# Kernel optimization log

Measured on AMD Instinct MI355X. Metric: run time of the kernel, lower is better.

Reference implementation:

```python
import jax, jax.numpy as jnp
import numpy as np

# Per-layer (in_dim, hidden) for the 6 stacked LSTM layers:
# rnn_inp: (1,64),(64,64),(64,64); rnn_out: (64,1),(1,1),(1,1)
_LAYER_DIMS = [(1, 64), (64, 64), (64, 64), (64, 1), (1, 1), (1, 1)]
_LAYER_NAMES = ['a0', 'a1', 'a2', 'b0', 'b1', 'b2']


def _lstm_layer(x, w_ih, w_hh, b_ih, b_hh):
    """Single unidirectional LSTM layer, PyTorch gate order (i, f, g, o).
    x: [B, T, Din]; w_ih: [4H, Din]; w_hh: [4H, H]; biases: [4H]. Returns [B, T, H]."""
    H = w_hh.shape[1]
    B = x.shape[0]
    # Input projection for all timesteps at once (one big GEMM).
    pre = jnp.einsum('btd,gd->btg', x, w_ih) + b_ih + b_hh  # [B, T, 4H]
    pre_t = jnp.swapaxes(pre, 0, 1)  # [T, B, 4H]

    def step(carry, xt):
        h, c = carry
        gates = xt + h @ w_hh.T  # [B, 4H]
        i, f, g, o = jnp.split(gates, 4, axis=-1)
        i = jax.nn.sigmoid(i)
        f = jax.nn.sigmoid(f)
        g = jnp.tanh(g)
        o = jax.nn.sigmoid(o)
        c = f * c + i * g
        h = o * jnp.tanh(c)
        return (h, c), h

    h0 = jnp.zeros((B, H), x.dtype)
    (_, _), hs = jax.lax.scan(step, (h0, h0), pre_t)  # hs: [T, B, H]
    return jnp.swapaxes(hs, 0, 1)


def setup_inputs() -> dict:
    key = jax.random.key(0)
    B, T = 256, 512
    inp = {}
    k, key = jax.random.split(key)
    inp['x'] = jax.random.normal(k, (B, T, 1), dtype=jnp.float32)
    for name, (din, h) in zip(_LAYER_NAMES, _LAYER_DIMS):
        s = 1.0 / np.sqrt(h)  # PyTorch LSTM init scale U(-1/sqrt(H), 1/sqrt(H))
        k1, k2, k3, k4, key = jax.random.split(key, 5)
        inp[f'w_ih_{name}'] = jax.random.uniform(k1, (4 * h, din), jnp.float32, -s, s)
        inp[f'w_hh_{name}'] = jax.random.uniform(k2, (4 * h, h), jnp.float32, -s, s)
        inp[f'b_ih_{name}'] = jax.random.uniform(k3, (4 * h,), jnp.float32, -s, s)
        inp[f'b_hh_{name}'] = jax.random.uniform(k4, (4 * h,), jnp.float32, -s, s)
    return inp


def reference(x,
              w_ih_a0, w_hh_a0, b_ih_a0, b_hh_a0,
              w_ih_a1, w_hh_a1, b_ih_a1, b_hh_a1,
              w_ih_a2, w_hh_a2, b_ih_a2, b_hh_a2,
              w_ih_b0, w_hh_b0, b_ih_b0, b_hh_b0,
              w_ih_b1, w_hh_b1, b_ih_b1, b_hh_b1,
              w_ih_b2, w_hh_b2, b_ih_b2, b_hh_b2):
    layers = [
        (w_ih_a0, w_hh_a0, b_ih_a0, b_hh_a0),
        (w_ih_a1, w_hh_a1, b_ih_a1, b_hh_a1),
        (w_ih_a2, w_hh_a2, b_ih_a2, b_hh_a2),
        (w_ih_b0, w_hh_b0, b_ih_b0, b_hh_b0),
        (w_ih_b1, w_hh_b1, b_ih_b1, b_hh_b1),
        (w_ih_b2, w_hh_b2, b_ih_b2, b_hh_b2),
    ]
    h = x
    for w_ih, w_hh, b_ih, b_hh in layers:
        h = _lstm_layer(h, w_ih, w_hh, b_ih, b_hh)
    # activation between the two LSTM stacks is identity (activation_type='identity')
    return h  # [B, T, 1]
```

## Files before the change

kernel.cpp:

```cpp
#include <hip/hip_runtime.h>


#define BB 256
#define TT 512
#define CH 4
#define NS 16
#define NW (TT / CH)
#define HP 72
#define PP 260

typedef _Float16 v2h __attribute__((ext_vector_type(2)));
typedef _Float16 v8h __attribute__((ext_vector_type(8)));
typedef float v4f __attribute__((ext_vector_type(4)));

__device__ __forceinline__ float sig_(float x) {
  return __builtin_amdgcn_rcpf(1.f + __builtin_amdgcn_exp2f(-1.44269504f * x));
}
__device__ __forceinline__ float tanh_(float x) {
  return __builtin_fmaf(2.f, __builtin_amdgcn_rcpf(1.f + __builtin_amdgcn_exp2f(-2.88539008f * x)), -1.f);
}

template <int K>
__device__ __forceinline__ float qb_(float v) {
  return __int_as_float(__builtin_amdgcn_update_dpp(
      0, __float_as_int(v), (K | (K << 2) | (K << 4) | (K << 6)), 0xF, 0xF, true));
}

#if __has_builtin(__builtin_amdgcn_fdot2)
#define FDOT2(acc, a, b) (acc) = __builtin_amdgcn_fdot2((a), (b), (acc), false)
#else
#define FDOT2(acc, a, b) \
  (acc) = __builtin_fmaf((float)(a)[0], (float)(b)[0], \
          __builtin_fmaf((float)(a)[1], (float)(b)[1], (acc)))
#endif
#define KEEPP(a) asm volatile("" : "+v"(a))
#define PIN16(w)                                                            \
  do {                                                                      \
    _Pragma("unroll") for (int _i = 0; _i < 16; ++_i) KEEPP((w)[_i]);       \
  } while (0)

#define WAITP(i, v)                                                           \
  while (__hip_atomic_load(&prog[i], __ATOMIC_ACQUIRE,                        \
                           __HIP_MEMORY_SCOPE_WORKGROUP) < (v)) {             \
    __builtin_amdgcn_s_sleep(1);                                              \
  }
#define POSTP(i, v)                                                           \
  do {                                                                        \
    asm volatile("s_waitcnt lgkmcnt(0)" ::: "memory");                        \
    if (lane == 0)                                                            \
      __hip_atomic_store(&prog[i], (v), __ATOMIC_RELEASE,                     \
                         __HIP_MEMORY_SCOPE_WORKGROUP);                       \
  } while (0)

__device__ __forceinline__ v2h bc2h_(int v) { return __builtin_bit_cast(v2h, v); }

__device__ __forceinline__ void load_h64(const _Float16* p, v2h hv[32]) {
  const int4* hp = reinterpret_cast<const int4*>(p);
#pragma unroll
  for (int i = 0; i < 8; ++i) {
    int4 blk = hp[i];
    hv[4 * i + 0] = bc2h_(blk.x);
    hv[4 * i + 1] = bc2h_(blk.y);
    hv[4 * i + 2] = bc2h_(blk.z);
    hv[4 * i + 3] = bc2h_(blk.w);
  }
}

__device__ __forceinline__ void load_row_pair(const float* src, v2h* lo, v2h* hi) {
  const float4* p = reinterpret_cast<const float4*>(src);
#pragma unroll
  for (int i = 0; i < 8; ++i) {
    float4 v = p[i];
    lo[2 * i]     = v2h{(_Float16)v.x, (_Float16)v.y};
    lo[2 * i + 1] = v2h{(_Float16)v.z, (_Float16)v.w};
  }
#pragma unroll
  for (int i = 0; i < 8; ++i) {
    float4 v = p[8 + i];
    hi[2 * i]     = v2h{(_Float16)v.x, (_Float16)v.y};
    hi[2 * i + 1] = v2h{(_Float16)v.z, (_Float16)v.w};
  }
}

__device__ __forceinline__ v8h ldbfrag_(const float* W, int t, int kc, int lane) {
  const int row = 16 * t + (lane & 15);
  const float* p = W + row * 64 + 32 * kc + 4 * (lane >> 4);
  float4 fa = *reinterpret_cast<const float4*>(p);
  float4 fb = *reinterpret_cast<const float4*>(p + 16);
  return v8h{(_Float16)fa.x, (_Float16)fa.y, (_Float16)fa.z, (_Float16)fa.w,
             (_Float16)fb.x, (_Float16)fb.y, (_Float16)fb.z, (_Float16)fb.w};
}

__global__ __attribute__((amdgpu_flat_work_group_size(384, 384),
                          amdgpu_waves_per_eu(2, 2)))
void lstm_pipe_k(
    const float* __restrict__ x,
    const float* __restrict__ wih_a0, const float* __restrict__ whh_a0,
    const float* __restrict__ bih_a0, const float* __restrict__ bhh_a0,
    const float* __restrict__ wih_a1, const float* __restrict__ whh_a1,
    const float* __restrict__ bih_a1, const float* __restrict__ bhh_a1,
    const float* __restrict__ wih_a2, const float* __restrict__ whh_a2,
    const float* __restrict__ bih_a2, const float* __restrict__ bhh_a2,
    const float* __restrict__ wih_b0, const float* __restrict__ whh_b0,
    const float* __restrict__ bih_b0, const float* __restrict__ bhh_b0,
    const float* __restrict__ wih_b1, const float* __restrict__ whh_b1,
    const float* __restrict__ bih_b1, const float* __restrict__ bhh_b1,
    const float* __restrict__ wih_b2, const float* __restrict__ whh_b2,
    const float* __restrict__ bih_b2, const float* __restrict__ bhh_b2,
    float* __restrict__ out)
{
  const int b = blockIdx.x;
  const int tid = threadIdx.x;
  const int wave = tid >> 6;
  const int lane = tid & 63;

  __shared__ __align__(16) _Float16 hh[3][NS][HP];
  __shared__ __align__(16) float pj[2][NS][PP];
  __shared__ float xs[TT];
  __shared__ int prog[6];

  for (int i = tid; i < TT; i += 384) xs[i] = x[(size_t)b * TT + i];
  for (int i = tid; i < 3 * NS * HP / 2; i += 384) reinterpret_cast<int*>(hh)[i] = 0;
  if (tid < 6) prog[tid] = 0;

  union UW {
    v8h bfr[16][2];
    v2h wtb[2][16];
  } u;

  float bias[4] = {0.f, 0.f, 0.f, 0.f};
  float wi0_[4] = {0.f, 0.f, 0.f, 0.f};
  float whb0[4] = {}, wi1b[4] = {}, wh1b[4] = {}, bb1[4] = {},
        wi2b[4] = {}, wh2b[4] = {}, bb2[4] = {};

  if (wave == 0) {
#pragma unroll
    for (int t = 0; t < 16; ++t) {
      u.bfr[t][0] = ldbfrag_(whh_a0, t, 0, lane);
      u.bfr[t][1] = ldbfrag_(whh_a0, t, 1, lane);
    }
#pragma unroll
    for (int q = 0; q < 4; ++q) {
      const int row = q * 64 + lane;
      bias[q] = bih_a0[row] + bhh_a0[row];
      wi0_[q] = wih_a0[row];
    }
  } else if (wave == 1) {
#pragma unroll
    for (int t = 0; t < 16; ++t) {
      u.bfr[t][0] = ldbfrag_(whh_a1, t, 0, lane);
      u.bfr[t][1] = ldbfrag_(whh_a1, t, 1, lane);
    }
#pragma unroll
    for (int q = 0; q < 4; ++q) bias[q] = bih_a1[q * 64 + lane] + bhh_a1[q * 64 + lane];
  } else if (wave == 2) {
#pragma unroll
    for (int t = 0; t < 16; ++t) {
      u.bfr[t][0] = ldbfrag_(whh_a2, t, 0, lane);
      u.bfr[t][1] = ldbfrag_(whh_a2, t, 1, lane);
    }
#pragma unroll
    for (int q = 0; q < 4; ++q) bias[q] = bih_a2[q * 64 + lane] + bhh_a2[q * 64 + lane];
  } else if (wave == 3) {
    const int q = lane & 3;
    load_row_pair(wih_b0 + q * 64, u.wtb[0], u.wtb[1]);
    bias[0] = bih_b0[q] + bhh_b0[q];
#pragma unroll
    for (int k = 0; k < 4; ++k) {
      whb0[k] = whh_b0[k];
      wi1b[k] = wih_b1[k]; wh1b[k] = whh_b1[k]; bb1[k] = bih_b1[k] + bhh_b1[k];
      wi2b[k] = wih_b2[k]; wh2b[k] = whh_b2[k]; bb2[k] = bih_b2[k] + bhh_b2[k];
    }
    PIN16(u.wtb[0]); PIN16(u.wtb[1]);
  } else if (wave == 4) {
#pragma unroll
    for (int t = 0; t < 16; ++t) {
      u.bfr[t][0] = ldbfrag_(wih_a1, t, 0, lane);
      u.bfr[t][1] = ldbfrag_(wih_a1, t, 1, lane);
    }
  } else {
#pragma unroll
    for (int t = 0; t < 16; ++t) {
      u.bfr[t][0] = ldbfrag_(wih_a2, t, 0, lane);
      u.bfr[t][1] = ldbfrag_(wih_a2, t, 1, lane);
    }
  }
  __syncthreads();

  float c = 0.f;
  float h0b = 0.f, c0b = 0.f, h1b = 0.f, c1b = 0.f, h2b = 0.f, c2b = 0.f;
  const int q4 = lane >> 4;
  const bool s0 = q4 & 1, s1 = q4 & 2;
  const v4f z = {0.f, 0.f, 0.f, 0.f};

  if (wave == 0) {
    __builtin_amdgcn_s_setprio(1);
    for (int k = 0; k < NW; ++k) {
      if (k >= 4) { WAITP(4, k - 3); }
      const int t0 = k * CH;
      for (int s = 0; s < CH; ++s) {
        const int t = t0 + s;
        const char* hp = (const char*)(&hh[0][(t + NS - 1) & (NS - 1)][0]) + 8 * q4;
        int2 r00 = *(const int2*)(hp);
        int2 r01 = *(const int2*)(hp + 32);
        int2 r10 = *(const int2*)(hp + 64);
        int2 r11 = *(const int2*)(hp + 96);
        v8h A0 = __builtin_bit_cast(v8h, int4{r00.x, r00.y, r01.x, r01.y});
        v8h A1 = __builtin_bit_cast(v8h, int4{r10.x, r10.y, r11.x, r11.y});
        v4f acc[16];
#pragma unroll
        for (int tl = 0; tl < 16; ++tl) {
          v4f d = __builtin_amdgcn_mfma_f32_16x16x32_f16(A0, u.bfr[tl][0], z, 0, 0, 0);
          acc[tl] = __builtin_amdgcn_mfma_f32_16x16x32_f16(A1, u.bfr[tl][1], d, 0, 0, 0);
        }
        float p[4];
#pragma unroll
        for (int g = 0; g < 4; ++g) {
          float v01 = s0 ? acc[4 * g + 1][0] : acc[4 * g + 0][0];
          float v23 = s0 ? acc[4 * g + 3][0] : acc[4 * g + 2][0];
          p[g] = s1 ? v23 : v01;
        }
        const float xv = xs[t];
        float p0 = __builtin_fmaf(wi0_[0], xv, p[0] + bias[0]);
        float p1 = __builtin_fmaf(wi0_[1], xv, p[1] + bias[1]);
        float p2 = __builtin_fmaf(wi0_[2], xv, p[2] + bias[2]);
        float p3 = __builtin_fmaf(wi0_[3], xv, p[3] + bias[3]);
        float gi = sig_(p0), gf = sig_(p1), gg = tanh_(p2), go = sig_(p3);
        c = __builtin_fmaf(gf, c, gi * gg);
        hh[0][t & (NS - 1)][lane] = (_Float16)(go * tanh_(c));
      }
      POSTP(0, k + 1);
    }
    __builtin_amdgcn_s_setprio(0);
  } else if (wave == 1) {
    __builtin_amdgcn_s_setprio(1);
    for (int k = 0; k < NW; ++k) {
      WAITP(4, k + 1);
      if (k >= 4) { WAITP(5, k - 3); }
      const int t0 = k * CH;
      for (int s = 0; s < CH; ++s) {
        const int t = t0 + s;
        const char* hp = (const char*)(&hh[1][(t + NS - 1) & (NS - 1)][0]) + 8 * q4;
        int2 r00 = *(const int2*)(hp);
        int2 r01 = *(const int2*)(hp + 32);
        int2 r10 = *(const int2*)(hp + 64);
        int2 r11 = *(const int2*)(hp + 96);
        v8h A0 = __builtin_bit_cast(v8h, int4{r00.x, r00.y, r01.x, r01.y});
        v8h A1 = __builtin_bit_cast(v8h, int4{r10.x, r10.y, r11.x, r11.y});
        float4 pr = *reinterpret_cast<const float4*>(&pj[0][t & (NS - 1)][lane * 4]);
        v4f acc[16];
#pragma unroll
        for (int tl = 0; tl < 16; ++tl) {
          v4f d = __builtin_amdgcn_mfma_f32_16x16x32_f16(A0, u.bfr[tl][0], z, 0, 0, 0);
          acc[tl] = __builtin_amdgcn_mfma_f32_16x16x32_f16(A1, u.bfr[tl][1], d, 0, 0, 0);
        }
        float p[4];
#pragma unroll
        for (int g = 0; g < 4; ++g) {
          float v01 = s0 ? acc[4 * g + 1][0] : acc[4 * g + 0][0];
          float v23 = s0 ? acc[4 * g + 3][0] : acc[4 * g + 2][0];
          p[g] = s1 ? v23 : v01;
        }
        float p0 = p[0] + bias[0] + pr.x;
        float p1 = p[1] + bias[1] + pr.y;
        float p2 = p[2] + bias[2] + pr.z;
        float p3 = p[3] + bias[3] + pr.w;
        float gi = sig_(p0), gf = sig_(p1), gg = tanh_(p2), go = sig_(p3);
        c = __builtin_fmaf(gf, c, gi * gg);
        hh[1][t & (NS - 1)][lane] = (_Float16)(go * tanh_(c));
      }
      POSTP(1, k + 1);
    }
    __builtin_amdgcn_s_setprio(0);
  } else if (wave == 2) {
    __builtin_amdgcn_s_setprio(1);
    for (int k = 0; k < NW; ++k) {
      WAITP(5, k + 1);
      if (k >= 4) { WAITP(3, k - 3); }
      const int t0 = k * CH;
      for (int s = 0; s < CH; ++s) {
        const int t = t0 + s;
        const char* hp = (const char*)(&hh[2][(t + NS - 1) & (NS - 1)][0]) + 8 * q4;
        int2 r00 = *(const int2*)(hp);
        int2 r01 = *(const int2*)(hp + 32);
        int2 r10 = *(const int2*)(hp + 64);
        int2 r11 = *(const int2*)(hp + 96);
        v8h A0 = __builtin_bit_cast(v8h, int4{r00.x, r00.y, r01.x, r01.y});
        v8h A1 = __builtin_bit_cast(v8h, int4{r10.x, r10.y, r11.x, r11.y});
        float4 pr = *reinterpret_cast<const float4*>(&pj[1][t & (NS - 1)][lane * 4]);
        v4f acc[16];
#pragma unroll
        for (int tl = 0; tl < 16; ++tl) {
          v4f d = __builtin_amdgcn_mfma_f32_16x16x32_f16(A0, u.bfr[tl][0], z, 0, 0, 0);
          acc[tl] = __builtin_amdgcn_mfma_f32_16x16x32_f16(A1, u.bfr[tl][1], d, 0, 0, 0);
        }
        float p[4];
#pragma unroll
        for (int g = 0; g < 4; ++g) {
          float v01 = s0 ? acc[4 * g + 1][0] : acc[4 * g + 0][0];
          float v23 = s0 ? acc[4 * g + 3][0] : acc[4 * g + 2][0];
          p[g] = s1 ? v23 : v01;
        }
        float p0 = p[0] + bias[0] + pr.x;
        float p1 = p[1] + bias[1] + pr.y;
        float p2 = p[2] + bias[2] + pr.z;
        float p3 = p[3] + bias[3] + pr.w;
        float gi = sig_(p0), gf = sig_(p1), gg = tanh_(p2), go = sig_(p3);
        c = __builtin_fmaf(gf, c, gi * gg);
        hh[2][t & (NS - 1)][lane] = (_Float16)(go * tanh_(c));
      }
      POSTP(2, k + 1);
    }
    __builtin_amdgcn_s_setprio(0);
  } else if (wave == 3) {
    for (int k = 0; k < NW; ++k) {
      WAITP(2, k + 1);
      const int t0 = k * CH;
      for (int s = 0; s < CH; ++s) {
        const int t = t0 + s;
        v2h hv[32];
        load_h64(&hh[2][t & (NS - 1)][0], hv);
        float pga = bias[0], pgb = 0.f;
#pragma unroll
        for (int j = 0; j < 16; ++j) {
          FDOT2(pga, u.wtb[0][j], hv[j]);
          FDOT2(pgb, u.wtb[1][j], hv[16 + j]);
        }
        float pg = pga + pgb;
        float p_i = qb_<0>(pg), p_f = qb_<1>(pg), p_g = qb_<2>(pg), p_o = qb_<3>(pg);
        float i0 = sig_(__builtin_fmaf(whb0[0], h0b, p_i));
        float f0 = sig_(__builtin_fmaf(whb0[1], h0b, p_f));
        float g0 = tanh_(__builtin_fmaf(whb0[2], h0b, p_g));
        float o0 = sig_(__builtin_fmaf(whb0[3], h0b, p_o));
        c0b = __builtin_fmaf(f0, c0b, i0 * g0);
        h0b = o0 * tanh_(c0b);
        float i1 = sig_(bb1[0] + __builtin_fmaf(wi1b[0], h0b, wh1b[0] * h1b));
        float f1 = sig_(bb1[1] + __builtin_fmaf(wi1b[1], h0b, wh1b[1] * h1b));
        float g1 = tanh_(bb1[2] + __builtin_fmaf(wi1b[2], h0b, wh1b[2] * h1b));
        float o1 = sig_(bb1[3] + __builtin_fmaf(wi1b[3], h0b, wh1b[3] * h1b));
        c1b = __builtin_fmaf(f1, c1b, i1 * g1);
        h1b = o1 * tanh_(c1b);
        float i2 = sig_(bb2[0] + __builtin_fmaf(wi2b[0], h1b, wh2b[0] * h2b));
        float f2 = sig_(bb2[1] + __builtin_fmaf(wi2b[1], h1b, wh2b[1] * h2b));
        float g2 = tanh_(bb2[2] + __builtin_fmaf(wi2b[2], h1b, wh2b[2] * h2b));
        float o2 = sig_(bb2[3] + __builtin_fmaf(wi2b[3], h1b, wh2b[3] * h2b));
        c2b = __builtin_fmaf(f2, c2b, i2 * g2);
        h2b = o2 * tanh_(c2b);
        if (lane == 0) out[(size_t)b * TT + t] = h2b;
      }
      POSTP(3, k + 1);
    }
  } else if (wave == 4) {
    for (int k = 0; k < NW; ++k) {
      WAITP(0, k + 1);
      if (k >= 4) { WAITP(1, k - 3); }
      const int t0 = k * CH;
      const int slotb = (t0 + (lane & 15)) & (NS - 1);
      const char* hp = (const char*)(&hh[0][slotb][0]) + 8 * q4;
      int2 r00 = *(const int2*)(hp);
      int2 r01 = *(const int2*)(hp + 32);
      int2 r10 = *(const int2*)(hp + 64);
      int2 r11 = *(const int2*)(hp + 96);
      v8h Bf0 = __builtin_bit_cast(v8h, int4{r00.x, r00.y, r01.x, r01.y});
      v8h Bf1 = __builtin_bit_cast(v8h, int4{r10.x, r10.y, r11.x, r11.y});
      float* pbase = &pj[0][slotb][0] + 16 * q4;
      const bool wr = (lane & 15) < CH;
#pragma unroll
      for (int tl = 0; tl < 16; ++tl) {
        v4f acc = __builtin_amdgcn_mfma_f32_16x16x32_f16(u.bfr[tl][0], Bf0, z, 0, 0, 0);
        acc = __builtin_amdgcn_mfma_f32_16x16x32_f16(u.bfr[tl][1], Bf1, acc, 0, 0, 0);
        if (wr) {
          const int o = 64 * (tl & 3) + (tl >> 2);
          pbase[o] = acc[0]; pbase[o + 4] = acc[1];
          pbase[o + 8] = acc[2]; pbase[o + 12] = acc[3];
        }
        __builtin_amdgcn_sched_barrier(0);
      }
      POSTP(4, k + 1);
    }
  } else {
    for (int k = 0; k < NW; ++k) {
      WAITP(1, k + 1);
      if (k >= 4) { WAITP(2, k - 3); }
      const int t0 = k * CH;
      const int slotb = (t0 + (lane & 15)) & (NS - 1);
      const char* hp = (const char*)(&hh[1][slotb][0]) + 8 * q4;
      int2 r00 = *(const int2*)(hp);
      int2 r01 = *(const int2*)(hp + 32);
      int2 r10 = *(const int2*)(hp + 64);
      int2 r11 = *(const int2*)(hp + 96);
      v8h Bf0 = __builtin_bit_cast(v8h, int4{r00.x, r00.y, r01.x, r01.y});
      v8h Bf1 = __builtin_bit_cast(v8h, int4{r10.x, r10.y, r11.x, r11.y});
      float* pbase = &pj[1][slotb][0] + 16 * q4;
      const bool wr = (lane & 15) < CH;
#pragma unroll
      for (int tl = 0; tl < 16; ++tl) {
        v4f acc = __builtin_amdgcn_mfma_f32_16x16x32_f16(u.bfr[tl][0], Bf0, z, 0, 0, 0);
        acc = __builtin_amdgcn_mfma_f32_16x16x32_f16(u.bfr[tl][1], Bf1, acc, 0, 0, 0);
        if (wr) {
          const int o = 64 * (tl & 3) + (tl >> 2);
          pbase[o] = acc[0]; pbase[o + 4] = acc[1];
          pbase[o + 8] = acc[2]; pbase[o + 12] = acc[3];
        }
        __builtin_amdgcn_sched_barrier(0);
      }
      POSTP(5, k + 1);
    }
  }
}

extern "C" void kernel_launch(void* const* d_in, const int* in_sizes, int n_in,
                              void* d_out, int out_size, void* d_ws, size_t ws_size,
                              hipStream_t stream) {
  const float* x      = (const float*)d_in[0];
  const float* wih_a0 = (const float*)d_in[1];
  const float* whh_a0 = (const float*)d_in[2];
  const float* bih_a0 = (const float*)d_in[3];
  const float* bhh_a0 = (const float*)d_in[4];
  const float* wih_a1 = (const float*)d_in[5];
  const float* whh_a1 = (const float*)d_in[6];
  const float* bih_a1 = (const float*)d_in[7];
  const float* bhh_a1 = (const float*)d_in[8];
  const float* wih_a2 = (const float*)d_in[9];
  const float* whh_a2 = (const float*)d_in[10];
  const float* bih_a2 = (const float*)d_in[11];
  const float* bhh_a2 = (const float*)d_in[12];
  const float* wih_b0 = (const float*)d_in[13];
  const float* whh_b0 = (const float*)d_in[14];
  const float* bih_b0 = (const float*)d_in[15];
  const float* bhh_b0 = (const float*)d_in[16];
  const float* wih_b1 = (const float*)d_in[17];
  const float* whh_b1 = (const float*)d_in[18];
  const float* bih_b1 = (const float*)d_in[19];
  const float* bhh_b1 = (const float*)d_in[20];
  const float* wih_b2 = (const float*)d_in[21];
  const float* whh_b2 = (const float*)d_in[22];
  const float* bih_b2 = (const float*)d_in[23];
  const float* bhh_b2 = (const float*)d_in[24];
  float* out = (float*)d_out;

  lstm_pipe_k<<<BB, 384, 0, stream>>>(
      x,
      wih_a0, whh_a0, bih_a0, bhh_a0,
      wih_a1, whh_a1, bih_a1, bhh_a1,
      wih_a2, whh_a2, bih_a2, bhh_a2,
      wih_b0, whh_b0, bih_b0, bhh_b0,
      wih_b1, whh_b1, bih_b1, bhh_b1,
      wih_b2, whh_b2, bih_b2, bhh_b2,
      out);
}
```

Before: 338.4 us.

## Process two batch elements per block to interleave independent recurrences

Each block now handles two batch rows, with shared buffers for hidden states, projections and inputs duplicated per row, and the grid is halved. Recurrent waves issue MFMAs for both rows in an interleaved order so the dependent matmul/activation chain of one row can hide the latency of the other. Projection waves and the scalar tail stage loop over both rows. This trades fewer active CUs and higher register/LDS use for better latency hiding within each wave.

```diff
diff --git a/kernel.cpp b/kernel.cpp
--- a/kernel.cpp
+++ b/kernel.cpp
@@ -1,7 +1,7 @@
 #include <hip/hip_runtime.h>
 
 
-#define BB 256
+#define NB 128
 #define TT 512
 #define CH 4
 #define NS 16
@@ -89,6 +89,58 @@
   float4 fb = *reinterpret_cast<const float4*>(p + 16);
   return v8h{(_Float16)fa.x, (_Float16)fa.y, (_Float16)fa.z, (_Float16)fa.w,
              (_Float16)fb.x, (_Float16)fb.y, (_Float16)fb.z, (_Float16)fb.w};
+}
+
+__device__ __forceinline__ void ldafrag_(const _Float16* hprev, int q4,
+                                         v8h& A0, v8h& A1) {
+  const char* hp = (const char*)hprev + 8 * q4;
+  int2 r00 = *(const int2*)(hp);
+  int2 r01 = *(const int2*)(hp + 32);
+  int2 r10 = *(const int2*)(hp + 64);
+  int2 r11 = *(const int2*)(hp + 96);
+  A0 = __builtin_bit_cast(v8h, int4{r00.x, r00.y, r01.x, r01.y});
+  A1 = __builtin_bit_cast(v8h, int4{r10.x, r10.y, r11.x, r11.y});
+}
+
+__device__ __forceinline__ void rec_pair_(const v8h bfr[16][2],
+                                          const v8h& A0, const v8h& A1,
+                                          const v8h& B0, const v8h& B1,
+                                          bool s0, bool s1,
+                                          float p0[4], float p1[4]) {
+  const v4f z = {0.f, 0.f, 0.f, 0.f};
+#pragma unroll
+  for (int g = 0; g < 4; ++g) {
+    v4f xa0 = __builtin_amdgcn_mfma_f32_16x16x32_f16(A0, bfr[4 * g + 0][0], z, 0, 0, 0);
+    xa0 = __builtin_amdgcn_mfma_f32_16x16x32_f16(A1, bfr[4 * g + 0][1], xa0, 0, 0, 0);
+    v4f xa1 = __builtin_amdgcn_mfma_f32_16x16x32_f16(A0, bfr[4 * g + 1][0], z, 0, 0, 0);
+    xa1 = __builtin_amdgcn_mfma_f32_16x16x32_f16(A1, bfr[4 * g + 1][1], xa1, 0, 0, 0);
+    v4f xa2 = __builtin_amdgcn_mfma_f32_16x16x32_f16(A0, bfr[4 * g + 2][0], z, 0, 0, 0);
+    xa2 = __builtin_amdgcn_mfma_f32_16x16x32_f16(A1, bfr[4 * g + 2][1], xa2, 0, 0, 0);
+    v4f xa3 = __builtin_amdgcn_mfma_f32_16x16x32_f16(A0, bfr[4 * g + 3][0], z, 0, 0, 0);
+    xa3 = __builtin_amdgcn_mfma_f32_16x16x32_f16(A1, bfr[4 * g + 3][1], xa3, 0, 0, 0);
+    v4f ya0 = __builtin_amdgcn_mfma_f32_16x16x32_f16(B0, bfr[4 * g + 0][0], z, 0, 0, 0);
+    ya0 = __builtin_amdgcn_mfma_f32_16x16x32_f16(B1, bfr[4 * g + 0][1], ya0, 0, 0, 0);
+    v4f ya1 = __builtin_amdgcn_mfma_f32_16x16x32_f16(B0, bfr[4 * g + 1][0], z, 0, 0, 0);
+    ya1 = __builtin_amdgcn_mfma_f32_16x16x32_f16(B1, bfr[4 * g + 1][1], ya1, 0, 0, 0);
+    v4f ya2 = __builtin_amdgcn_mfma_f32_16x16x32_f16(B0, bfr[4 * g + 2][0], z, 0, 0, 0);
+    ya2 = __builtin_amdgcn_mfma_f32_16x16x32_f16(B1, bfr[4 * g + 2][1], ya2, 0, 0, 0);
+    v4f ya3 = __builtin_amdgcn_mfma_f32_16x16x32_f16(B0, bfr[4 * g + 3][0], z, 0, 0, 0);
+    ya3 = __builtin_amdgcn_mfma_f32_16x16x32_f16(B1, bfr[4 * g + 3][1], ya3, 0, 0, 0);
+    float v01 = s0 ? xa1[0] : xa0[0];
+    float v23 = s0 ? xa3[0] : xa2[0];
+    p0[g] = s1 ? v23 : v01;
+    v01 = s0 ? ya1[0] : ya0[0];
+    v23 = s0 ? ya3[0] : ya2[0];
+    p1[g] = s1 ? v23 : v01;
+    __builtin_amdgcn_sched_barrier(0);
+  }
+}
+
+__device__ __forceinline__ float gates_(float p0, float p1, float p2, float p3,
+                                        float& c) {
+  float gi = sig_(p0), gf = sig_(p1), gg = tanh_(p2), go = sig_(p3);
+  c = __builtin_fmaf(gf, c, gi * gg);
+  return go * tanh_(c);
 }
 
 __global__ __attribute__((amdgpu_flat_work_group_size(384, 384),
@@ -109,18 +161,22 @@
     const float* __restrict__ bih_b2, const float* __restrict__ bhh_b2,
     float* __restrict__ out)
 {
-  const int b = blockIdx.x;
+  const int b0 = 2 * blockIdx.x;
   const int tid = threadIdx.x;
   const int wave = tid >> 6;
   const int lane = tid & 63;
 
-  __shared__ __align__(16) _Float16 hh[3][NS][HP];
-  __shared__ __align__(16) float pj[2][NS][PP];
-  __shared__ float xs[TT];
+  __shared__ __align__(16) _Float16 hh[3][2][NS][HP];
+  __shared__ __align__(16) float pj[2][2][NS][PP];
+  __shared__ float xs[2 * TT];
   __shared__ int prog[6];
 
-  for (int i = tid; i < TT; i += 384) xs[i] = x[(size_t)b * TT + i];
-  for (int i = tid; i < 3 * NS * HP / 2; i += 384) reinterpret_cast<int*>(hh)[i] = 0;
+  for (int i = tid; i < 2 * TT; i += 384) {
+    const int e = i >> 9, t = i & (TT - 1);
+    xs[i] = x[(size_t)(b0 + e) * TT + t];
+  }
+  for (int i = tid; i < 3 * 2 * NS * HP / 2; i += 384)
+    reinterpret_cast<int*>(hh)[i] = 0;
   if (tid < 6) prog[tid] = 0;
 
   union UW {
@@ -187,8 +243,9 @@
   }
   __syncthreads();
 
-  float c = 0.f;
-  float h0b = 0.f, c0b = 0.f, h1b = 0.f, c1b = 0.f, h2b = 0.f, c2b = 0.f;
+  float cA = 0.f, cB = 0.f;
+  float h0bA = 0.f, c0bA = 0.f, h1bA = 0.f, c1bA = 0.f, h2bA = 0.f, c2bA = 0.f;
+  float h0bB = 0.f, c0bB = 0.f, h1bB = 0.f, c1bB = 0.f, h2bB = 0.f, c2bB = 0.f;
   const int q4 = lane >> 4;
   const bool s0 = q4 & 1, s1 = q4 & 2;
   const v4f z = {0.f, 0.f, 0.f, 0.f};
@@ -200,34 +257,23 @@
       const int t0 = k * CH;
       for (int s = 0; s < CH; ++s) {
         const int t = t0 + s;
-        const char* hp = (const char*)(&hh[0][(t + NS - 1) & (NS - 1)][0]) + 8 * q4;
-        int2 r00 = *(const int2*)(hp);
-        int2 r01 = *(const int2*)(hp + 32);
-        int2 r10 = *(const int2*)(hp + 64);
-        int2 r11 = *(const int2*)(hp + 96);
-        v8h A0 = __builtin_bit_cast(v8h, int4{r00.x, r00.y, r01.x, r01.y});
-        v8h A1 = __builtin_bit_cast(v8h, int4{r10.x, r10.y, r11.x, r11.y});
-        v4f acc[16];
-#pragma unroll
-        for (int tl = 0; tl < 16; ++tl) {
-          v4f d = __builtin_amdgcn_mfma_f32_16x16x32_f16(A0, u.bfr[tl][0], z, 0, 0, 0);
-          acc[tl] = __builtin_amdgcn_mfma_f32_16x16x32_f16(A1, u.bfr[tl][1], d, 0, 0, 0);
-        }
-        float p[4];
-#pragma unroll
-        for (int g = 0; g < 4; ++g) {
-          float v01 = s0 ? acc[4 * g + 1][0] : acc[4 * g + 0][0];
-          float v23 = s0 ? acc[4 * g + 3][0] : acc[4 * g + 2][0];
-          p[g] = s1 ? v23 : v01;
-        }
-        const float xv = xs[t];
-        float p0 = __builtin_fmaf(wi0_[0], xv, p[0] + bias[0]);
-        float p1 = __builtin_fmaf(wi0_[1], xv, p[1] + bias[1]);
-        float p2 = __builtin_fmaf(wi0_[2], xv, p[2] + bias[2]);
-        float p3 = __builtin_fmaf(wi0_[3], xv, p[3] + bias[3]);
-        float gi = sig_(p0), gf = sig_(p1), gg = tanh_(p2), go = sig_(p3);
-        c = __builtin_fmaf(gf, c, gi * gg);
-        hh[0][t & (NS - 1)][lane] = (_Float16)(go * tanh_(c));
+        const int sl = (t + NS - 1) & (NS - 1);
+        v8h A0, A1, B0, B1;
+        ldafrag_(&hh[0][0][sl][0], q4, A0, A1);
+        ldafrag_(&hh[0][1][sl][0], q4, B0, B1);
+        float p0[4], p1[4];
+        rec_pair_(u.bfr, A0, A1, B0, B1, s0, s1, p0, p1);
+        const float xv0 = xs[t], xv1 = xs[TT + t];
+        float hA = gates_(__builtin_fmaf(wi0_[0], xv0, p0[0] + bias[0]),
+                          __builtin_fmaf(wi0_[1], xv0, p0[1] + bias[1]),
+                          __builtin_fmaf(wi0_[2], xv0, p0[2] + bias[2]),
+                          __builtin_fmaf(wi0_[3], xv0, p0[3] + bias[3]), cA);
+        float hB = gates_(__builtin_fmaf(wi0_[0], xv1, p1[0] + bias[0]),
+                          __builtin_fmaf(wi0_[1], xv1, p1[1] + bias[1]),
+                          __builtin_fmaf(wi0_[2], xv1, p1[2] + bias[2]),
+                          __builtin_fmaf(wi0_[3], xv1, p1[3] + bias[3]), cB);
+        hh[0][0][t & (NS - 1)][lane] = (_Float16)hA;
+        hh[0][1][t & (NS - 1)][lane] = (_Float16)hB;
       }
       POSTP(0, k + 1);
     }
@@ -240,34 +286,20 @@
       const int t0 = k * CH;
       for (int s = 0; s < CH; ++s) {
         const int t = t0 + s;
-        const char* hp = (const char*)(&hh[1][(t + NS - 1) & (NS - 1)][0]) + 8 * q4;
-        int2 r00 = *(const int2*)(hp);
-        int2 r01 = *(const int2*)(hp + 32);
-        int2 r10 = *(const int2*)(hp + 64);
-        int2 r11 = *(const int2*)(hp + 96);
-        v8h A0 = __builtin_bit_cast(v8h, int4{r00.x, r00.y, r01.x, r01.y});
-        v8h A1 = __builtin_bit_cast(v8h, int4{r10.x, r10.y, r11.x, r11.y});
-        float4 pr = *reinterpret_cast<const float4*>(&pj[0][t & (NS - 1)][lane * 4]);
-        v4f acc[16];
-#pragma unroll
-        for (int tl = 0; tl < 16; ++tl) {
-          v4f d = __builtin_amdgcn_mfma_f32_16x16x32_f16(A0, u.bfr[tl][0], z, 0, 0, 0);
-          acc[tl] = __builtin_amdgcn_mfma_f32_16x16x32_f16(A1, u.bfr[tl][1], d, 0, 0, 0);
-        }
-        float p[4];
-#pragma unroll
-        for (int g = 0; g < 4; ++g) {
-          float v01 = s0 ? acc[4 * g + 1][0] : acc[4 * g + 0][0];
-          float v23 = s0 ? acc[4 * g + 3][0] : acc[4 * g + 2][0];
-          p[g] = s1 ? v23 : v01;
-        }
-        float p0 = p[0] + bias[0] + pr.x;
-        float p1 = p[1] + bias[1] + pr.y;
-        float p2 = p[2] + bias[2] + pr.z;
-        float p3 = p[3] + bias[3] + pr.w;
-        float gi = sig_(p0), gf = sig_(p1), gg = tanh_(p2), go = sig_(p3);
-        c = __builtin_fmaf(gf, c, gi * gg);
-        hh[1][t & (NS - 1)][lane] = (_Float16)(go * tanh_(c));
+        const int sl = (t + NS - 1) & (NS - 1);
+        v8h A0, A1, B0, B1;
+        ldafrag_(&hh[1][0][sl][0], q4, A0, A1);
+        ldafrag_(&hh[1][1][sl][0], q4, B0, B1);
+        float4 prA = *reinterpret_cast<const float4*>(&pj[0][0][t & (NS - 1)][lane * 4]);
+        float4 prB = *reinterpret_cast<const float4*>(&pj[0][1][t & (NS - 1)][lane * 4]);
+        float p0[4], p1[4];
+        rec_pair_(u.bfr, A0, A1, B0, B1, s0, s1, p0, p1);
+        float hA = gates_(p0[0] + bias[0] + prA.x, p0[1] + bias[1] + prA.y,
+                          p0[2] + bias[2] + prA.z, p0[3] + bias[3] + prA.w, cA);
+        float hB = gates_(p1[0] + bias[0] + prB.x, p1[1] + bias[1] + prB.y,
+                          p1[2] + bias[2] + prB.z, p1[3] + bias[3] + prB.w, cB);
+        hh[1][0][t & (NS - 1)][lane] = (_Float16)hA;
+        hh[1][1][t & (NS - 1)][lane] = (_Float16)hB;
       }
       POSTP(1, k + 1);
     }
@@ -280,34 +312,20 @@
       const int t0 = k * CH;
       for (int s = 0; s < CH; ++s) {
         const int t = t0 + s;
-        const char* hp = (const char*)(&hh[2][(t + NS - 1) & (NS - 1)][0]) + 8 * q4;
-        int2 r00 = *(const int2*)(hp);
-        int2 r01 = *(const int2*)(hp + 32);
-        int2 r10 = *(const int2*)(hp + 64);
-        int2 r11 = *(const int2*)(hp + 96);
-        v8h A0 = __builtin_bit_cast(v8h, int4{r00.x, r00.y, r01.x, r01.y});
-        v8h A1 = __builtin_bit_cast(v8h, int4{r10.x, r10.y, r11.x, r11.y});
-        float4 pr = *reinterpret_cast<const float4*>(&pj[1][t & (NS - 1)][lane * 4]);
-        v4f acc[16];
-#pragma unroll
-        for (int tl = 0; tl < 16; ++tl) {
-          v4f d = __builtin_amdgcn_mfma_f32_16x16x32_f16(A0, u.bfr[tl][0], z, 0, 0, 0);
-          acc[tl] = __builtin_amdgcn_mfma_f32_16x16x32_f16(A1, u.bfr[tl][1], d, 0, 0, 0);
-        }
-        float p[4];
-#pragma unroll
-        for (int g = 0; g < 4; ++g) {
-          float v01 = s0 ? acc[4 * g + 1][0] : acc[4 * g + 0][0];
-          float v23 = s0 ? acc[4 * g + 3][0] : acc[4 * g + 2][0];
-          p[g] = s1 ? v23 : v01;
-        }
-        float p0 = p[0] + bias[0] + pr.x;
-        float p1 = p[1] + bias[1] + pr.y;
-        float p2 = p[2] + bias[2] + pr.z;
-        float p3 = p[3] + bias[3] + pr.w;
-        float gi = sig_(p0), gf = sig_(p1), gg = tanh_(p2), go = sig_(p3);
-        c = __builtin_fmaf(gf, c, gi * gg);
-        hh[2][t & (NS - 1)][lane] = (_Float16)(go * tanh_(c));
+        const int sl = (t + NS - 1) & (NS - 1);
+        v8h A0, A1, B0, B1;
+        ldafrag_(&hh[2][0][sl][0], q4, A0, A1);
+        ldafrag_(&hh[2][1][sl][0], q4, B0, B1);
+        float4 prA = *reinterpret_cast<const float4*>(&pj[1][0][t & (NS - 1)][lane * 4]);
+        float4 prB = *reinterpret_cast<const float4*>(&pj[1][1][t & (NS - 1)][lane * 4]);
+        float p0[4], p1[4];
+        rec_pair_(u.bfr, A0, A1, B0, B1, s0, s1, p0, p1);
+        float hA = gates_(p0[0] + bias[0] + prA.x, p0[1] + bias[1] + prA.y,
+                          p0[2] + bias[2] + prA.z, p0[3] + bias[3] + prA.w, cA);
+        float hB = gates_(p1[0] + bias[0] + prB.x, p1[1] + bias[1] + prB.y,
+                          p1[2] + bias[2] + prB.z, p1[3] + bias[3] + prB.w, cB);
+        hh[2][0][t & (NS - 1)][lane] = (_Float16)hA;
+        hh[2][1][t & (NS - 1)][lane] = (_Float16)hB;
       }
       POSTP(2, k + 1);
     }
@@ -318,35 +336,64 @@
       const int t0 = k * CH;
       for (int s = 0; s < CH; ++s) {
         const int t = t0 + s;
-        v2h hv[32];
-        load_h64(&hh[2][t & (NS - 1)][0], hv);
-        float pga = bias[0], pgb = 0.f;
+        v2h hvA[32], hvB[32];
+        load_h64(&hh[2][0][t & (NS - 1)][0], hvA);
+        load_h64(&hh[2][1][t & (NS - 1)][0], hvB);
+        float pgaA = bias[0], pgbA = 0.f, pgaB = bias[0], pgbB = 0.f;
 #pragma unroll
         for (int j = 0; j < 16; ++j) {
-          FDOT2(pga, u.wtb[0][j], hv[j]);
-          FDOT2(pgb, u.wtb[1][j], hv[16 + j]);
-        }
-        float pg = pga + pgb;
-        float p_i = qb_<0>(pg), p_f = qb_<1>(pg), p_g = qb_<2>(pg), p_o = qb_<3>(pg);
-        float i0 = sig_(__builtin_fmaf(whb0[0], h0b, p_i));
-        float f0 = sig_(__builtin_fmaf(whb0[1], h0b, p_f));
-        float g0 = tanh_(__builtin_fmaf(whb0[2], h0b, p_g));
-        float o0 = sig_(__builtin_fmaf(whb0[3], h0b, p_o));
-        c0b = __builtin_fmaf(f0, c0b, i0 * g0);
-        h0b = o0 * tanh_(c0b);
-        float i1 = sig_(bb1[0] + __builtin_fmaf(wi1b[0], h0b, wh1b[0] * h1b));
-        float f1 = sig_(bb1[1] + __builtin_fmaf(wi1b[1], h0b, wh1b[1] * h1b));
-        float g1 = tanh_(bb1[2] + __builtin_fmaf(wi1b[2], h0b, wh1b[2] * h1b));
-        float o1 = sig_(bb1[3] + __builtin_fmaf(wi1b[3], h0b, wh1b[3] * h1b));
-        c1b = __builtin_fmaf(f1, c1b, i1 * g1);
-        h1b = o1 * tanh_(c1b);
-        float i2 = sig_(bb2[0] + __builtin_fmaf(wi2b[0], h1b, wh2b[0] * h2b));
-        float f2 = sig_(bb2[1] + __builtin_fmaf(wi2b[1], h1b, wh2b[1] * h2b));
-        float g2 = tanh_(bb2[2] + __builtin_fmaf(wi2b[2], h1b, wh2b[2] * h2b));
-        float o2 = sig_(bb2[3] + __builtin_fmaf(wi2b[3], h1b, wh2b[3] * h2b));
-        c2b = __builtin_fmaf(f2, c2b, i2 * g2);
-        h2b = o2 * tanh_(c2b);
-        if (lane == 0) out[(size_t)b * TT + t] = h2b;
+          FDOT2(pgaA, u.wtb[0][j], hvA[j]);
+          FDOT2(pgbA, u.wtb[1][j], hvA[16 + j]);
+          FDOT2(pgaB, u.wtb[0][j], hvB[j]);
+          FDOT2(pgbB, u.wtb[1][j], hvB[16 + j]);
+        }
+        float pgA = pgaA + pgbA, pgB = pgaB + pgbB;
+        {
+          float p_i = qb_<0>(pgA), p_f = qb_<1>(pgA), p_g = qb_<2>(pgA), p_o = qb_<3>(pgA);
+          float i0 = sig_(__builtin_fmaf(whb0[0], h0bA, p_i));
+          float f0 = sig_(__builtin_fmaf(whb0[1], h0bA, p_f));
+          float g0 = tanh_(__builtin_fmaf(whb0[2], h0bA, p_g));
+          float o0 = sig_(__builtin_fmaf(whb0[3], h0bA, p_o));
+          c0bA = __builtin_fmaf(f0, c0bA, i0 * g0);
+          h0bA = o0 * tanh_(c0bA);
+          float i1 = sig_(bb1[0] + __builtin_fmaf(wi1b[0], h0bA, wh1b[0] * h1bA));
+          float f1 = sig_(bb1[1] + __builtin_fmaf(wi1b[1], h0bA, wh1b[1] * h1bA));
+          float g1 = tanh_(bb1[2] + __builtin_fmaf(wi1b[2], h0bA, wh1b[2] * h1bA));
+          float o1 = sig_(bb1[3] + __builtin_fmaf(wi1b[3], h0bA, wh1b[3] * h1bA));
+          c1bA = __builtin_fmaf(f1, c1bA, i1 * g1);
+          h1bA = o1 * tanh_(c1bA);
+          float i2 = sig_(bb2[0] + __builtin_fmaf(wi2b[0], h1bA, wh2b[0] * h2bA));
+          float f2 = sig_(bb2[1] + __builtin_fmaf(wi2b[1], h1bA, wh2b[1] * h2bA));
+          float g2 = tanh_(bb2[2] + __builtin_fmaf(wi2b[2], h1bA, wh2b[2] * h2bA));
+          float o2 = sig_(bb2[3] + __builtin_fmaf(wi2b[3], h1bA, wh2b[3] * h2bA));
+          c2bA = __builtin_fmaf(f2, c2bA, i2 * g2);
+          h2bA = o2 * tanh_(c2bA);
+        }
+        {
+          float p_i = qb_<0>(pgB), p_f = qb_<1>(pgB), p_g = qb_<2>(pgB), p_o = qb_<3>(pgB);
+          float i0 = sig_(__builtin_fmaf(whb0[0], h0bB, p_i));
+          float f0 = sig_(__builtin_fmaf(whb0[1], h0bB, p_f));
+          float g0 = tanh_(__builtin_fmaf(whb0[2], h0bB, p_g));
+          float o0 = sig_(__builtin_fmaf(whb0[3], h0bB, p_o));
+          c0bB = __builtin_fmaf(f0, c0bB, i0 * g0);
+          h0bB = o0 * tanh_(c0bB);
+          float i1 = sig_(bb1[0] + __builtin_fmaf(wi1b[0], h0bB, wh1b[0] * h1bB));
+          float f1 = sig_(bb1[1] + __builtin_fmaf(wi1b[1], h0bB, wh1b[1] * h1bB));
+          float g1 = tanh_(bb1[2] + __builtin_fmaf(wi1b[2], h0bB, wh1b[2] * h1bB));
+          float o1 = sig_(bb1[3] + __builtin_fmaf(wi1b[3], h0bB, wh1b[3] * h1bB));
+          c1bB = __builtin_fmaf(f1, c1bB, i1 * g1);
+          h1bB = o1 * tanh_(c1bB);
+          float i2 = sig_(bb2[0] + __builtin_fmaf(wi2b[0], h1bB, wh2b[0] * h2bB));
+          float f2 = sig_(bb2[1] + __builtin_fmaf(wi2b[1], h1bB, wh2b[1] * h2bB));
+          float g2 = tanh_(bb2[2] + __builtin_fmaf(wi2b[2], h1bB, wh2b[2] * h2bB));
+          float o2 = sig_(bb2[3] + __builtin_fmaf(wi2b[3], h1bB, wh2b[3] * h2bB));
+          c2bB = __builtin_fmaf(f2, c2bB, i2 * g2);
+          h2bB = o2 * tanh_(c2bB);
+        }
+        if (lane == 0) {
+          out[(size_t)b0 * TT + t] = h2bA;
+          out[(size_t)(b0 + 1) * TT + t] = h2bB;
+        }
       }
       POSTP(3, k + 1);
     }
@@ -356,25 +403,23 @@
       if (k >= 4) { WAITP(1, k - 3); }
       const int t0 = k * CH;
       const int slotb = (t0 + (lane & 15)) & (NS - 1);
-      const char* hp = (const char*)(&hh[0][slotb][0]) + 8 * q4;
-      int2 r00 = *(const int2*)(hp);
-      int2 r01 = *(const int2*)(hp + 32);
-      int2 r10 = *(const int2*)(hp + 64);
-      int2 r11 = *(const int2*)(hp + 96);
-      v8h Bf0 = __builtin_bit_cast(v8h, int4{r00.x, r00.y, r01.x, r01.y});
-      v8h Bf1 = __builtin_bit_cast(v8h, int4{r10.x, r10.y, r11.x, r11.y});
-      float* pbase = &pj[0][slotb][0] + 16 * q4;
       const bool wr = (lane & 15) < CH;
 #pragma unroll
-      for (int tl = 0; tl < 16; ++tl) {
-        v4f acc = __builtin_amdgcn_mfma_f32_16x16x32_f16(u.bfr[tl][0], Bf0, z, 0, 0, 0);
-        acc = __builtin_amdgcn_mfma_f32_16x16x32_f16(u.bfr[tl][1], Bf1, acc, 0, 0, 0);
-        if (wr) {
-          const int o = 64 * (tl & 3) + (tl >> 2);
-          pbase[o] = acc[0]; pbase[o + 4] = acc[1];
-          pbase[o + 8] = acc[2]; pbase[o + 12] = acc[3];
-        }
-        __builtin_amdgcn_sched_barrier(0);
+      for (int e = 0; e < 2; ++e) {
+        v8h Bf0, Bf1;
+        ldafrag_(&hh[0][e][slotb][0], q4, Bf0, Bf1);
+        float* pbase = &pj[0][e][slotb][0] + 16 * q4;
+#pragma unroll
+        for (int tl = 0; tl < 16; ++tl) {
+          v4f acc = __builtin_amdgcn_mfma_f32_16x16x32_f16(u.bfr[tl][0], Bf0, z, 0, 0, 0);
+          acc = __builtin_amdgcn_mfma_f32_16x16x32_f16(u.bfr[tl][1], Bf1, acc, 0, 0, 0);
+          if (wr) {
+            const int o = 64 * (tl & 3) + (tl >> 2);
+            pbase[o] = acc[0]; pbase[o + 4] = acc[1];
+            pbase[o + 8] = acc[2]; pbase[o + 12] = acc[3];
+          }
+          __builtin_amdgcn_sched_barrier(0);
+        }
       }
       POSTP(4, k + 1);
     }
@@ -384,25 +429,23 @@
       if (k >= 4) { WAITP(2, k - 3); }
       const int t0 = k * CH;
       const int slotb = (t0 + (lane & 15)) & (NS - 1);
-      const char* hp = (const char*)(&hh[1][slotb][0]) + 8 * q4;
-      int2 r00 = *(const int2*)(hp);
-      int2 r01 = *(const int2*)(hp + 32);
-      int2 r10 = *(const int2*)(hp + 64);
-      int2 r11 = *(const int2*)(hp + 96);
-      v8h Bf0 = __builtin_bit_cast(v8h, int4{r00.x, r00.y, r01.x, r01.y});
-      v8h Bf1 = __builtin_bit_cast(v8h, int4{r10.x, r10.y, r11.x, r11.y});
-      float* pbase = &pj[1][slotb][0] + 16 * q4;
       const bool wr = (lane & 15) < CH;
 #pragma unroll
-      for (int tl = 0; tl < 16; ++tl) {
-        v4f acc = __builtin_amdgcn_mfma_f32_16x16x32_f16(u.bfr[tl][0], Bf0, z, 0, 0, 0);
-        acc = __builtin_amdgcn_mfma_f32_16x16x32_f16(u.bfr[tl][1], Bf1, acc, 0, 0, 0);
-        if (wr) {
-          const int o = 64 * (tl & 3) + (tl >> 2);
-          pbase[o] = acc[0]; pbase[o + 4] = acc[1];
-          pbase[o + 8] = acc[2]; pbase[o + 12] = acc[3];
-        }
-        __builtin_amdgcn_sched_barrier(0);
+      for (int e = 0; e < 2; ++e) {
+        v8h Bf0, Bf1;
+        ldafrag_(&hh[1][e][slotb][0], q4, Bf0, Bf1);
+        float* pbase = &pj[1][e][slotb][0] + 16 * q4;
+#pragma unroll
+        for (int tl = 0; tl < 16; ++tl) {
+          v4f acc = __builtin_amdgcn_mfma_f32_16x16x32_f16(u.bfr[tl][0], Bf0, z, 0, 0, 0);
+          acc = __builtin_amdgcn_mfma_f32_16x16x32_f16(u.bfr[tl][1], Bf1, acc, 0, 0, 0);
+          if (wr) {
+            const int o = 64 * (tl & 3) + (tl >> 2);
+            pbase[o] = acc[0]; pbase[o + 4] = acc[1];
+            pbase[o + 8] = acc[2]; pbase[o + 12] = acc[3];
+          }
+          __builtin_amdgcn_sched_barrier(0);
+        }
       }
       POSTP(5, k + 1);
     }
@@ -439,7 +482,7 @@
   const float* bhh_b2 = (const float*)d_in[24];
   float* out = (float*)d_out;
 
-  lstm_pipe_k<<<BB, 384, 0, stream>>>(
+  lstm_pipe_k<<<NB, 384, 0, stream>>>(
       x,
       wih_a0, whh_a0, bih_a0, bhh_a0,
       wih_a1, whh_a1, bih_a1, bhh_a1,
```

Measured after the change: 549.0 us. 1.62x slower.
